# Performance work log

Measured on AMD Instinct MI355X. Metric: run time of the kernel, lower is better.

The kernel has to match this reference:

```python
import jax, jax.numpy as jnp
import numpy as np

SCALE = 8.0  # sqrt(d_head=64), per init_kwargs
B, H, S, D = 2, 16, 2048, 64


def setup_inputs() -> dict:
    key = jax.random.key(0)
    kq, kk, kv = jax.random.split(key, 3)
    q = jax.random.normal(kq, (B, H, S, D), dtype=jnp.float32)
    k = jax.random.normal(kk, (B, H, S, D), dtype=jnp.float32)
    v = jax.random.normal(kv, (B, H, S, D), dtype=jnp.float32)
    # causal mask: True where attention is NOT allowed (strictly upper triangle)
    causal = jnp.triu(jnp.ones((S, S), dtype=bool), k=1)
    mask = jnp.broadcast_to(causal, (B, H, S, S))
    return {"q": q, "k": k, "v": v, "mask": mask}


def reference(q, k, v, mask):
    # score = (q @ k^T) / scale, masked_fill(mask, -inf), softmax, @ v
    score = jnp.einsum('bhqd,bhkd->bhqk', q, k) / SCALE
    score = jnp.where(mask, -jnp.inf, score)
    attn = jax.nn.softmax(score, axis=-1)
    output = jnp.einsum('bhqk,bhkd->bhqd', attn, v)
    return (attn, output)
```

## Files before the change

### kernel.cpp

```cpp
#include <hip/hip_runtime.h>
#include <hip/hip_bf16.h>

#define S_LEN 2048
#define D_HEAD 64
#define SD (S_LEN * D_HEAD)
#define TILE_B 8192
#define NTILES 32

typedef __attribute__((ext_vector_type(8))) short short8;
typedef __attribute__((ext_vector_type(4))) float f32x4;

__device__ __forceinline__ unsigned short f2b(float f) {
  unsigned int u = __float_as_uint(f);
  u += 0x7fffu + ((u >> 16) & 1u);
  return (unsigned short)(u >> 16);
}

__device__ __forceinline__ float b2f(unsigned short s) {
  return __uint_as_float(((unsigned int)s) << 16);
}

__device__ __forceinline__ void gl_lds16(const void* g, void* l) {
  __builtin_amdgcn_global_load_lds(
      (const __attribute__((address_space(1))) unsigned int*)g,
      (__attribute__((address_space(3))) unsigned int*)l, 16, 0, 0);
}

__device__ __forceinline__ void stage8k(const char* gsrc, char* ldst, int w, int lane) {
  gl_lds16(gsrc + ((w * 64 + lane) << 4),        ldst + ((w * 64) << 4));
  gl_lds16(gsrc + ((256 + w * 64 + lane) << 4),  ldst + ((256 + w * 64) << 4));
}

__global__ __launch_bounds__(256) void convert_kv_kernel(
    const float* __restrict__ K, const float* __restrict__ V,
    char* __restrict__ Kpre, char* __restrict__ Vpre) {
  const int bid = blockIdx.x;
  const int tid = threadIdx.x;
  if (bid < 1024) {
    const int bh = bid >> 5, tile = bid & 31;
    const float* Kb = K + (size_t)bh * SD + tile * 64 * 64;
    char* out = Kpre + (size_t)bid * TILE_B;
    #pragma unroll
    for (int j = 0; j < 2; ++j) {
      int c = tid + j * 256;
      int sl = c >> 3;
      int d0 = ((c & 7) ^ (sl & 7)) << 3;
      const float* src = Kb + sl * 64 + d0;
      float4 a = *(const float4*)src;
      float4 b = *(const float4*)(src + 4);
      short8 o;
      o[0]=(short)f2b(a.x); o[1]=(short)f2b(a.y); o[2]=(short)f2b(a.z); o[3]=(short)f2b(a.w);
      o[4]=(short)f2b(b.x); o[5]=(short)f2b(b.y); o[6]=(short)f2b(b.z); o[7]=(short)f2b(b.w);
      *(short8*)(out + c * 16) = o;
    }
  } else {
    __shared__ float Vl[64][65];
    const int vb = bid - 1024;
    const int bh = vb >> 5, tile = vb & 31;
    const float* Vb = V + (size_t)bh * SD + tile * 64 * 64;
    #pragma unroll
    for (int j = 0; j < 4; ++j) {
      int row = (tid >> 4) + j * 16;
      int c4 = (tid & 15) << 2;
      float4 v = *(const float4*)(Vb + row * 64 + c4);
      Vl[row][c4+0] = v.x; Vl[row][c4+1] = v.y; Vl[row][c4+2] = v.z; Vl[row][c4+3] = v.w;
    }
    __syncthreads();
    char* out = Vpre + (size_t)vb * TILE_B;
    #pragma unroll
    for (int j = 0; j < 2; ++j) {
      int c = tid + j * 256;
      int d = c >> 3;
      int s0 = ((c & 7) ^ ((d >> 2) & 7)) << 3;
      short8 o;
      #pragma unroll
      for (int i = 0; i < 8; ++i) o[i] = (short)f2b(Vl[s0 + i][d]);
      *(short8*)(out + c * 16) = o;
    }
  }
}

__global__ __launch_bounds__(256, 4) void sdpa_pre_kernel(
    const float* __restrict__ Qg, const char* __restrict__ Kpre,
    const char* __restrict__ Vpre, float* __restrict__ attn,
    float* __restrict__ outp) {
  const int j  = blockIdx.x >> 8;
  const int rr = blockIdx.x & 255;
  const int xcd = rr & 7;
  const int cu  = rr >> 3;
  const int bh  = xcd + ((cu & 3) << 3);
  const int u   = cu >> 2;
  const int qt  = (j == 0) ? u : (j == 1) ? (15 - u) : (j == 2) ? (16 + u) : (31 - u);

  const int tid = threadIdx.x, wave = tid >> 6, lane = tid & 63;
  const int g = lane >> 4, m = lane & 15;
  const int swzK = (m & 7) << 4;

  __shared__ __align__(16) unsigned short Ring[4][4096];
  __shared__ __align__(16) unsigned short Pl[4][1024];
  char* const RB = (char*)Ring;
  char* const PB = (char*)(&Pl[wave][0]);

  const size_t bhSD = (size_t)bh * SD;
  const size_t bhSS = (size_t)bh << 22;
  const char* KpreBH = Kpre + (size_t)bh * NTILES * TILE_B;
  const char* VpreBH = Vpre + (size_t)bh * NTILES * TILE_B;

  int vro[4], vsz[4];
  #pragma unroll
  for (int dc = 0; dc < 4; ++dc) {
    int d = dc * 16 + m;
    vro[dc] = d << 7;
    vsz[dc] = ((d >> 2) & 7) << 4;
  }
  const float SCL = 0.18033688011112042f;

  const int q0 = qt << 6;
  const int nIt = qt + 1;
  const int qwrow = q0 + wave * 16;
  const int qbase = qwrow + g * 4;

  short8 aq0, aq1;
  {
    const float* qp = Qg + bhSD + (size_t)(qwrow + m) * D_HEAD + g * 8;
    float4 x0 = *(const float4*)(qp);
    float4 x1 = *(const float4*)(qp + 4);
    float4 y0 = *(const float4*)(qp + 32);
    float4 y1 = *(const float4*)(qp + 36);
    aq0[0]=(short)f2b(x0.x*SCL); aq0[1]=(short)f2b(x0.y*SCL);
    aq0[2]=(short)f2b(x0.z*SCL); aq0[3]=(short)f2b(x0.w*SCL);
    aq0[4]=(short)f2b(x1.x*SCL); aq0[5]=(short)f2b(x1.y*SCL);
    aq0[6]=(short)f2b(x1.z*SCL); aq0[7]=(short)f2b(x1.w*SCL);
    aq1[0]=(short)f2b(y0.x*SCL); aq1[1]=(short)f2b(y0.y*SCL);
    aq1[2]=(short)f2b(y0.z*SCL); aq1[3]=(short)f2b(y0.w*SCL);
    aq1[4]=(short)f2b(y1.x*SCL); aq1[5]=(short)f2b(y1.y*SCL);
    aq1[6]=(short)f2b(y1.z*SCL); aq1[7]=(short)f2b(y1.w*SCL);
  }

  float rs0 = 0.f, rs1 = 0.f, rs2 = 0.f, rs3 = 0.f;
  {
    const int npre = nIt < 3 ? nIt : 3;
    for (int t0 = 0; t0 < npre; ++t0)
      stage8k(KpreBH + (size_t)t0 * TILE_B, RB + t0 * TILE_B, wave, lane);
  }
  for (int it = 0; it < nIt; ++it) {
    if (it + 2 < nIt)      { asm volatile("s_waitcnt vmcnt(4)" ::: "memory"); }
    else if (it + 1 < nIt) { asm volatile("s_waitcnt vmcnt(2)" ::: "memory"); }
    else                   { asm volatile("s_waitcnt vmcnt(0)" ::: "memory"); }
    __builtin_amdgcn_s_barrier();
    __builtin_amdgcn_sched_barrier(0);
    if (it + 3 < nIt)
      stage8k(KpreBH + (size_t)(it + 3) * TILE_B, RB + ((it + 3) & 3) * TILE_B, wave, lane);
    asm volatile("" ::: "memory");
    const char* KB = RB + (it & 3) * TILE_B;
    const int kc = it << 6;
    if (kc + 64 <= qwrow) {
      #pragma unroll
      for (int t = 0; t < 4; ++t) {
        f32x4 acc = {0.f, 0.f, 0.f, 0.f};
        const int rb = (t * 16 + m) << 7;
        short8 b0 = *(const short8*)(KB + ((rb + g * 16) ^ swzK));
        short8 b1 = *(const short8*)(KB + ((rb + 64 + g * 16) ^ swzK));
        acc = __builtin_amdgcn_mfma_f32_16x16x32_bf16(aq0, b0, acc, 0, 0, 0);
        acc = __builtin_amdgcn_mfma_f32_16x16x32_bf16(aq1, b1, acc, 0, 0, 0);
        rs0 += exp2f(acc[0]);
        rs1 += exp2f(acc[1]);
        rs2 += exp2f(acc[2]);
        rs3 += exp2f(acc[3]);
      }
    } else {
      #pragma unroll
      for (int t = 0; t < 4; ++t) {
        f32x4 acc = {0.f, 0.f, 0.f, 0.f};
        const int rb = (t * 16 + m) << 7;
        short8 b0 = *(const short8*)(KB + ((rb + g * 16) ^ swzK));
        short8 b1 = *(const short8*)(KB + ((rb + 64 + g * 16) ^ swzK));
        acc = __builtin_amdgcn_mfma_f32_16x16x32_bf16(aq0, b0, acc, 0, 0, 0);
        acc = __builtin_amdgcn_mfma_f32_16x16x32_bf16(aq1, b1, acc, 0, 0, 0);
        const int kcol = kc + t * 16 + m;
        rs0 += (kcol <= qbase + 0) ? exp2f(acc[0]) : 0.f;
        rs1 += (kcol <= qbase + 1) ? exp2f(acc[1]) : 0.f;
        rs2 += (kcol <= qbase + 2) ? exp2f(acc[2]) : 0.f;
        rs3 += (kcol <= qbase + 3) ? exp2f(acc[3]) : 0.f;
      }
    }
  }
  #pragma unroll
  for (int sft = 1; sft < 16; sft <<= 1) {
    rs0 += __shfl_xor(rs0, sft, 64);
    rs1 += __shfl_xor(rs1, sft, 64);
    rs2 += __shfl_xor(rs2, sft, 64);
    rs3 += __shfl_xor(rs3, sft, 64);
  }
  const float ri0 = 1.f / rs0, ri1 = 1.f / rs1, ri2 = 1.f / rs2, ri3 = 1.f / rs3;

  f32x4 o0 = {0.f,0.f,0.f,0.f}, o1 = {0.f,0.f,0.f,0.f};
  f32x4 o2 = {0.f,0.f,0.f,0.f}, o3 = {0.f,0.f,0.f,0.f};
  __builtin_amdgcn_s_barrier();
  stage8k(KpreBH, RB + 0 * TILE_B, wave, lane);
  stage8k(VpreBH, RB + 2 * TILE_B, wave, lane);
  int cur = 0;
  const int r4 = lane >> 4;
  const int cf = (lane & 15) << 2;
  for (int it = 0; it < nIt; ++it) {
    if (it == 0) { asm volatile("s_waitcnt vmcnt(0)" ::: "memory"); }
    else         { asm volatile("s_waitcnt vmcnt(4)" ::: "memory"); }
    __builtin_amdgcn_s_barrier();
    __builtin_amdgcn_sched_barrier(0);
    if (it + 1 < nIt) {
      stage8k(KpreBH + (size_t)(it + 1) * TILE_B, RB + (cur ^ 1) * TILE_B, wave, lane);
      stage8k(VpreBH + (size_t)(it + 1) * TILE_B, RB + (2 + (cur ^ 1)) * TILE_B, wave, lane);
    }
    asm volatile("" ::: "memory");
    const char* KB = RB + cur * TILE_B;
    const char* VB = RB + (2 + cur) * TILE_B;
    const int kc = it << 6;
    if (kc + 64 <= qwrow) {
      #pragma unroll
      for (int t = 0; t < 4; ++t) {
        f32x4 acc = {0.f, 0.f, 0.f, 0.f};
        const int rb = (t * 16 + m) << 7;
        short8 b0 = *(const short8*)(KB + ((rb + g * 16) ^ swzK));
        short8 b1 = *(const short8*)(KB + ((rb + 64 + g * 16) ^ swzK));
        acc = __builtin_amdgcn_mfma_f32_16x16x32_bf16(aq0, b0, acc, 0, 0, 0);
        acc = __builtin_amdgcn_mfma_f32_16x16x32_bf16(aq1, b1, acc, 0, 0, 0);
        float p0 = exp2f(acc[0]) * ri0;
        float p1 = exp2f(acc[1]) * ri1;
        float p2 = exp2f(acc[2]) * ri2;
        float p3 = exp2f(acc[3]) * ri3;
        const int r0 = g * 4, c2 = (t * 16 + m) << 1;
        *(unsigned short*)(PB + ((((r0+0)<<7) + c2) ^ (((r0+0)&7)<<4))) = f2b(p0);
        *(unsigned short*)(PB + ((((r0+1)<<7) + c2) ^ (((r0+1)&7)<<4))) = f2b(p1);
        *(unsigned short*)(PB + ((((r0+2)<<7) + c2) ^ (((r0+2)&7)<<4))) = f2b(p2);
        *(unsigned short*)(PB + ((((r0+3)<<7) + c2) ^ (((r0+3)&7)<<4))) = f2b(p3);
      }
    } else {
      #pragma unroll
      for (int t = 0; t < 4; ++t) {
        f32x4 acc = {0.f, 0.f, 0.f, 0.f};
        const int rb = (t * 16 + m) << 7;
        short8 b0 = *(const short8*)(KB + ((rb + g * 16) ^ swzK));
        short8 b1 = *(const short8*)(KB + ((rb + 64 + g * 16) ^ swzK));
        acc = __builtin_amdgcn_mfma_f32_16x16x32_bf16(aq0, b0, acc, 0, 0, 0);
        acc = __builtin_amdgcn_mfma_f32_16x16x32_bf16(aq1, b1, acc, 0, 0, 0);
        const int kcol = kc + t * 16 + m;
        float p0 = (kcol <= qbase + 0) ? exp2f(acc[0]) * ri0 : 0.f;
        float p1 = (kcol <= qbase + 1) ? exp2f(acc[1]) * ri1 : 0.f;
        float p2 = (kcol <= qbase + 2) ? exp2f(acc[2]) * ri2 : 0.f;
        float p3 = (kcol <= qbase + 3) ? exp2f(acc[3]) * ri3 : 0.f;
        const int r0 = g * 4, c2 = (t * 16 + m) << 1;
        *(unsigned short*)(PB + ((((r0+0)<<7) + c2) ^ (((r0+0)&7)<<4))) = f2b(p0);
        *(unsigned short*)(PB + ((((r0+1)<<7) + c2) ^ (((r0+1)&7)<<4))) = f2b(p1);
        *(unsigned short*)(PB + ((((r0+2)<<7) + c2) ^ (((r0+2)&7)<<4))) = f2b(p2);
        *(unsigned short*)(PB + ((((r0+3)<<7) + c2) ^ (((r0+3)&7)<<4))) = f2b(p3);
      }
    }
    {
      float* abase2 = attn + bhSS + (size_t)qwrow * S_LEN + kc;
      #pragma unroll
      for (int jj = 0; jj < 4; ++jj) {
        const int row = 4 * jj + r4;
        const int off = (((row << 7) + (cf << 1))) ^ ((row & 7) << 4);
        ushort4 pr = *(const ushort4*)(PB + off);
        float4 fa;
        fa.x = b2f(pr.x); fa.y = b2f(pr.y); fa.z = b2f(pr.z); fa.w = b2f(pr.w);
        *(float4*)(abase2 + (size_t)row * S_LEN + cf) = fa;
      }
    }
    short8 pa0 = *(const short8*)(PB + (((m << 7) + g * 16) ^ swzK));
    short8 pa1 = *(const short8*)(PB + (((m << 7) + 64 + g * 16) ^ swzK));
    #pragma unroll
    for (int dc = 0; dc < 4; ++dc) {
      short8 bv0 = *(const short8*)(VB + ((vro[dc] + g * 16) ^ vsz[dc]));
      short8 bv1 = *(const short8*)(VB + ((vro[dc] + 64 + g * 16) ^ vsz[dc]));
      f32x4& od = (dc == 0) ? o0 : (dc == 1) ? o1 : (dc == 2) ? o2 : o3;
      od = __builtin_amdgcn_mfma_f32_16x16x32_bf16(pa0, bv0, od, 0, 0, 0);
      od = __builtin_amdgcn_mfma_f32_16x16x32_bf16(pa1, bv1, od, 0, 0, 0);
    }
    cur ^= 1;
  }

  #pragma unroll
  for (int reg = 0; reg < 4; ++reg) {
    float* op = outp + bhSD + (size_t)(qbase + reg) * D_HEAD + m;
    op[ 0] = o0[reg];
    op[16] = o1[reg];
    op[32] = o2[reg];
    op[48] = o3[reg];
  }

  const int col0 = nIt << 6;
  const int nvec = (S_LEN - col0) >> 2;
  if (nvec > 0) {
    const float4 z = {0.f, 0.f, 0.f, 0.f};
    for (int r = 0; r < 64; ++r) {
      float4* rp = (float4*)(attn + bhSS + (size_t)(q0 + r) * S_LEN + col0);
      for (int i = tid; i < nvec; i += 256) rp[i] = z;
    }
  }
}

__global__ __launch_bounds__(256) void sdpa_fb_kernel(
    const float* __restrict__ Qg, const float* __restrict__ Kg,
    const float* __restrict__ Vg, float* __restrict__ attn,
    float* __restrict__ outp) {
  const int bh = blockIdx.x >> 4;
  const int pi = blockIdx.x & 15;
  const int tid  = threadIdx.x;
  const int wave = tid >> 6;
  const int lane = tid & 63;
  const int g = lane >> 4;
  const int m = lane & 15;
  const int swzK = (m & 7) << 4;
  __shared__ __align__(16) unsigned short Kl[2][64 * 64];
  __shared__ __align__(16) unsigned short Vt[2][64 * 64];
  __shared__ __align__(16) unsigned short Pl[4][16 * 64];
  char* const PB = (char*)(&Pl[wave][0]);
  const size_t bhSD = (size_t)bh * (S_LEN * D_HEAD);
  const size_t bhSS = (size_t)bh * ((size_t)S_LEN * S_LEN);
  int ss[4], dd[4], koff[4];
  #pragma unroll
  for (int j = 0; j < 4; ++j) {
    int f = tid + j * 256;
    ss[j] = f >> 4;
    dd[j] = (f & 15) << 2;
    koff[j] = (((ss[j] << 6) + dd[j]) << 1) ^ ((ss[j] & 7) << 4);
  }
  int vro[4], vsz[4];
  #pragma unroll
  for (int dc = 0; dc < 4; ++dc) {
    int d = dc * 16 + m;
    vro[dc] = d << 7;
    vsz[dc] = ((d >> 2) & 7) << 4;
  }
  const float SCL = 0.18033688011112042f;
  for (int sidx = 0; sidx < 2; ++sidx) {
    const int qt = sidx ? (31 - pi) : pi;
    const int q0 = qt << 6;
    const int kmax = q0 + 64;
    const int nIter = kmax >> 6;
    const int qwrow = q0 + wave * 16;
    const int qbase = qwrow + g * 4;
    short8 aq0, aq1;
    {
      const float* qp = Qg + bhSD + (size_t)(qwrow + m) * D_HEAD + g * 8;
      float4 x0 = *(const float4*)(qp);
      float4 x1 = *(const float4*)(qp + 4);
      float4 y0 = *(const float4*)(qp + 32);
      float4 y1 = *(const float4*)(qp + 36);
      aq0[0]=(short)f2b(x0.x*SCL); aq0[1]=(short)f2b(x0.y*SCL);
      aq0[2]=(short)f2b(x0.z*SCL); aq0[3]=(short)f2b(x0.w*SCL);
      aq0[4]=(short)f2b(x1.x*SCL); aq0[5]=(short)f2b(x1.y*SCL);
      aq0[6]=(short)f2b(x1.z*SCL); aq0[7]=(short)f2b(x1.w*SCL);
      aq1[0]=(short)f2b(y0.x*SCL); aq1[1]=(short)f2b(y0.y*SCL);
      aq1[2]=(short)f2b(y0.z*SCL); aq1[3]=(short)f2b(y0.w*SCL);
      aq1[4]=(short)f2b(y1.x*SCL); aq1[5]=(short)f2b(y1.y*SCL);
      aq1[6]=(short)f2b(y1.z*SCL); aq1[7]=(short)f2b(y1.w*SCL);
    }
    float rs0 = 0.f, rs1 = 0.f, rs2 = 0.f, rs3 = 0.f;
    {
      float4 kr[4];
      #pragma unroll
      for (int j = 0; j < 4; ++j)
        kr[j] = *(const float4*)(Kg + bhSD + (size_t)ss[j] * D_HEAD + dd[j]);
      #pragma unroll
      for (int j = 0; j < 4; ++j) {
        ushort4 kb;
        kb.x = f2b(kr[j].x); kb.y = f2b(kr[j].y);
        kb.z = f2b(kr[j].z); kb.w = f2b(kr[j].w);
        *(ushort4*)((char*)Kl[0] + koff[j]) = kb;
      }
    }
    __syncthreads();
    int cur = 0;
    for (int it = 0; it < nIter; ++it) {
      const int kc = it << 6;
      const bool pf = (it + 1 < nIter);
      float4 kr[4];
      if (pf) {
        #pragma unroll
        for (int j = 0; j < 4; ++j)
          kr[j] = *(const float4*)(Kg + bhSD + (size_t)(kc + 64 + ss[j]) * D_HEAD + dd[j]);
      }
      const char* KB = (const char*)Kl[cur];
      #pragma unroll
      for (int t = 0; t < 4; ++t) {
        f32x4 acc = {0.f, 0.f, 0.f, 0.f};
        const int rb = (t * 16 + m) << 7;
        short8 b0 = *(const short8*)(KB + ((rb + g * 16) ^ swzK));
        short8 b1 = *(const short8*)(KB + ((rb + 64 + g * 16) ^ swzK));
        acc = __builtin_amdgcn_mfma_f32_16x16x32_bf16(aq0, b0, acc, 0, 0, 0);
        acc = __builtin_amdgcn_mfma_f32_16x16x32_bf16(aq1, b1, acc, 0, 0, 0);
        const int kcol = kc + t * 16 + m;
        rs0 += (kcol <= qbase + 0) ? exp2f(acc[0]) : 0.f;
        rs1 += (kcol <= qbase + 1) ? exp2f(acc[1]) : 0.f;
        rs2 += (kcol <= qbase + 2) ? exp2f(acc[2]) : 0.f;
        rs3 += (kcol <= qbase + 3) ? exp2f(acc[3]) : 0.f;
      }
      if (pf) {
        #pragma unroll
        for (int j = 0; j < 4; ++j) {
          ushort4 kb;
          kb.x = f2b(kr[j].x); kb.y = f2b(kr[j].y);
          kb.z = f2b(kr[j].z); kb.w = f2b(kr[j].w);
          *(ushort4*)((char*)Kl[cur ^ 1] + koff[j]) = kb;
        }
      }
      __syncthreads();
      cur ^= 1;
    }
    #pragma unroll
    for (int sft = 1; sft < 16; sft <<= 1) {
      rs0 += __shfl_xor(rs0, sft, 64);
      rs1 += __shfl_xor(rs1, sft, 64);
      rs2 += __shfl_xor(rs2, sft, 64);
      rs3 += __shfl_xor(rs3, sft, 64);
    }
    const float ri0 = 1.f / rs0, ri1 = 1.f / rs1, ri2 = 1.f / rs2, ri3 = 1.f / rs3;
    f32x4 o0 = {0.f,0.f,0.f,0.f}, o1 = {0.f,0.f,0.f,0.f};
    f32x4 o2 = {0.f,0.f,0.f,0.f}, o3 = {0.f,0.f,0.f,0.f};
    {
      float4 kr[4], vr[4];
      #pragma unroll
      for (int j = 0; j < 4; ++j) {
        kr[j] = *(const float4*)(Kg + bhSD + (size_t)ss[j] * D_HEAD + dd[j]);
        vr[j] = *(const float4*)(Vg + bhSD + (size_t)ss[j] * D_HEAD + dd[j]);
      }
      #pragma unroll
      for (int j = 0; j < 4; ++j) {
        ushort4 kb;
        kb.x = f2b(kr[j].x); kb.y = f2b(kr[j].y);
        kb.z = f2b(kr[j].z); kb.w = f2b(kr[j].w);
        *(ushort4*)((char*)Kl[0] + koff[j]) = kb;
        const int d0 = dd[j], s2 = ss[j] << 1;
        char* VB1 = (char*)Vt[0];
        *(unsigned short*)(VB1 + ((((d0+0)<<7) + s2) ^ ((((d0+0)>>2)&7)<<4))) = f2b(vr[j].x);
        *(unsigned short*)(VB1 + ((((d0+1)<<7) + s2) ^ ((((d0+1)>>2)&7)<<4))) = f2b(vr[j].y);
        *(unsigned short*)(VB1 + ((((d0+2)<<7) + s2) ^ ((((d0+2)>>2)&7)<<4))) = f2b(vr[j].z);
        *(unsigned short*)(VB1 + ((((d0+3)<<7) + s2) ^ ((((d0+3)>>2)&7)<<4))) = f2b(vr[j].w);
      }
    }
    __syncthreads();
    cur = 0;
    for (int it = 0; it < nIter; ++it) {
      const int kc = it << 6;
      const bool pf = (it + 1 < nIter);
      float4 kr[4], vr[4];
      if (pf) {
        #pragma unroll
        for (int j = 0; j < 4; ++j) {
          kr[j] = *(const float4*)(Kg + bhSD + (size_t)(kc + 64 + ss[j]) * D_HEAD + dd[j]);
          vr[j] = *(const float4*)(Vg + bhSD + (size_t)(kc + 64 + ss[j]) * D_HEAD + dd[j]);
        }
      }
      const char* KB = (const char*)Kl[cur];
      const char* VB = (const char*)Vt[cur];
      float* arow = attn + bhSS + (size_t)qbase * S_LEN + kc;
      #pragma unroll
      for (int t = 0; t < 4; ++t) {
        f32x4 acc = {0.f, 0.f, 0.f, 0.f};
        const int rb = (t * 16 + m) << 7;
        short8 b0 = *(const short8*)(KB + ((rb + g * 16) ^ swzK));
        short8 b1 = *(const short8*)(KB + ((rb + 64 + g * 16) ^ swzK));
        acc = __builtin_amdgcn_mfma_f32_16x16x32_bf16(aq0, b0, acc, 0, 0, 0);
        acc = __builtin_amdgcn_mfma_f32_16x16x32_bf16(aq1, b1, acc, 0, 0, 0);
        const int kcol = kc + t * 16 + m;
        const int tc = t * 16 + m;
        float p0 = (kcol <= qbase + 0) ? exp2f(acc[0]) * ri0 : 0.f;
        float p1 = (kcol <= qbase + 1) ? exp2f(acc[1]) * ri1 : 0.f;
        float p2 = (kcol <= qbase + 2) ? exp2f(acc[2]) * ri2 : 0.f;
        float p3 = (kcol <= qbase + 3) ? exp2f(acc[3]) * ri3 : 0.f;
        arow[0 * S_LEN + tc] = p0;
        arow[1 * S_LEN + tc] = p1;
        arow[2 * S_LEN + tc] = p2;
        arow[3 * S_LEN + tc] = p3;
        const int r0 = g * 4, c2 = tc << 1;
        *(unsigned short*)(PB + ((((r0+0)<<7) + c2) ^ (((r0+0)&7)<<4))) = f2b(p0);
        *(unsigned short*)(PB + ((((r0+1)<<7) + c2) ^ (((r0+1)&7)<<4))) = f2b(p1);
        *(unsigned short*)(PB + ((((r0+2)<<7) + c2) ^ (((r0+2)&7)<<4))) = f2b(p2);
        *(unsigned short*)(PB + ((((r0+3)<<7) + c2) ^ (((r0+3)&7)<<4))) = f2b(p3);
      }
      short8 pa0 = *(const short8*)(PB + (((m << 7) + g * 16) ^ swzK));
      short8 pa1 = *(const short8*)(PB + (((m << 7) + 64 + g * 16) ^ swzK));
      #pragma unroll
      for (int dc = 0; dc < 4; ++dc) {
        short8 bv0 = *(const short8*)(VB + ((vro[dc] + g * 16) ^ vsz[dc]));
        short8 bv1 = *(const short8*)(VB + ((vro[dc] + 64 + g * 16) ^ vsz[dc]));
        f32x4& od = (dc == 0) ? o0 : (dc == 1) ? o1 : (dc == 2) ? o2 : o3;
        od = __builtin_amdgcn_mfma_f32_16x16x32_bf16(pa0, bv0, od, 0, 0, 0);
        od = __builtin_amdgcn_mfma_f32_16x16x32_bf16(pa1, bv1, od, 0, 0, 0);
      }
      if (pf) {
        #pragma unroll
        for (int j = 0; j < 4; ++j) {
          ushort4 kb;
          kb.x = f2b(kr[j].x); kb.y = f2b(kr[j].y);
          kb.z = f2b(kr[j].z); kb.w = f2b(kr[j].w);
          *(ushort4*)((char*)Kl[cur ^ 1] + koff[j]) = kb;
          const int d0 = dd[j], s2 = ss[j] << 1;
          char* VB1 = (char*)Vt[cur ^ 1];
          *(unsigned short*)(VB1 + ((((d0+0)<<7) + s2) ^ ((((d0+0)>>2)&7)<<4))) = f2b(vr[j].x);
          *(unsigned short*)(VB1 + ((((d0+1)<<7) + s2) ^ ((((d0+1)>>2)&7)<<4))) = f2b(vr[j].y);
          *(unsigned short*)(VB1 + ((((d0+2)<<7) + s2) ^ ((((d0+2)>>2)&7)<<4))) = f2b(vr[j].z);
          *(unsigned short*)(VB1 + ((((d0+3)<<7) + s2) ^ ((((d0+3)>>2)&7)<<4))) = f2b(vr[j].w);
        }
      }
      __syncthreads();
      cur ^= 1;
    }
    #pragma unroll
    for (int reg = 0; reg < 4; ++reg) {
      float* op = outp + bhSD + (size_t)(qbase + reg) * D_HEAD + m;
      op[ 0] = o0[reg];
      op[16] = o1[reg];
      op[32] = o2[reg];
      op[48] = o3[reg];
    }
    const int ncols = S_LEN - kmax;
    if (ncols > 0) {
      const float4 z = {0.f, 0.f, 0.f, 0.f};
      const int nvec = ncols >> 2;
      for (int r = 0; r < 64; ++r) {
        float4* rp = (float4*)(attn + bhSS + (size_t)(q0 + r) * S_LEN + kmax);
        for (int i = tid; i < nvec; i += 256) rp[i] = z;
      }
    }
  }
}

extern "C" void kernel_launch(void* const* d_in, const int* in_sizes, int n_in,
                              void* d_out, int out_size, void* d_ws, size_t ws_size,
                              hipStream_t stream) {
  (void)in_sizes; (void)n_in; (void)out_size;
  const float* q = (const float*)d_in[0];
  const float* k = (const float*)d_in[1];
  const float* v = (const float*)d_in[2];
  float* attn = (float*)d_out;
  float* outp = attn + (size_t)2 * 16 * 2048 * 2048;
  const size_t pre_bytes = (size_t)32 * NTILES * TILE_B;
  if (ws_size >= 2 * pre_bytes) {
    char* Kpre = (char*)d_ws;
    char* Vpre = Kpre + pre_bytes;
    convert_kv_kernel<<<2048, 256, 0, stream>>>(k, v, Kpre, Vpre);
    sdpa_pre_kernel<<<1024, 256, 0, stream>>>(q, Kpre, Vpre, attn, outp);
  } else {
    sdpa_fb_kernel<<<512, 256, 0, stream>>>(q, k, v, attn, outp);
  }
}
```

Before: 168.6 us.

## Read K directly from global memory in row-sum pass instead of LDS ring

The first (softmax denominator) pass now loads pre-swizzled K fragments straight from global memory into registers, with precomputed per-lane offsets and a 2x unrolled loop. This drops the 4-slot LDS ring, the vmcnt waits and the workgroup barriers from that pass. The second pass keeps LDS double buffering, now in separate K and V arrays. The risk is exposed global/L2 latency without explicit prefetch, plus uncoalesced 16-byte per-lane loads repeated by all four waves.

```diff
diff --git a/kernel.cpp b/kernel.cpp
--- a/kernel.cpp
+++ b/kernel.cpp
@@ -96,9 +96,9 @@
   const int g = lane >> 4, m = lane & 15;
   const int swzK = (m & 7) << 4;
 
-  __shared__ __align__(16) unsigned short Ring[4][4096];
+  __shared__ __align__(16) unsigned short Kl[2][4096];
+  __shared__ __align__(16) unsigned short Vt[2][4096];
   __shared__ __align__(16) unsigned short Pl[4][1024];
-  char* const RB = (char*)Ring;
   char* const PB = (char*)(&Pl[wave][0]);
 
   const size_t bhSD = (size_t)bh * SD;
@@ -137,32 +137,28 @@
     aq1[6]=(short)f2b(y1.z*SCL); aq1[7]=(short)f2b(y1.w*SCL);
   }
 
+  int koffs[8];
+  #pragma unroll
+  for (int tt = 0; tt < 4; ++tt) {
+    const int s = tt * 16 + m;
+    const int sw = (s & 7) << 4;
+    koffs[2 * tt]     = (s << 7) + ((g * 16) ^ sw);
+    koffs[2 * tt + 1] = (s << 7) + ((64 + g * 16) ^ sw);
+  }
   float rs0 = 0.f, rs1 = 0.f, rs2 = 0.f, rs3 = 0.f;
-  {
-    const int npre = nIt < 3 ? nIt : 3;
-    for (int t0 = 0; t0 < npre; ++t0)
-      stage8k(KpreBH + (size_t)t0 * TILE_B, RB + t0 * TILE_B, wave, lane);
-  }
+  #pragma unroll 2
   for (int it = 0; it < nIt; ++it) {
-    if (it + 2 < nIt)      { asm volatile("s_waitcnt vmcnt(4)" ::: "memory"); }
-    else if (it + 1 < nIt) { asm volatile("s_waitcnt vmcnt(2)" ::: "memory"); }
-    else                   { asm volatile("s_waitcnt vmcnt(0)" ::: "memory"); }
-    __builtin_amdgcn_s_barrier();
-    __builtin_amdgcn_sched_barrier(0);
-    if (it + 3 < nIt)
-      stage8k(KpreBH + (size_t)(it + 3) * TILE_B, RB + ((it + 3) & 3) * TILE_B, wave, lane);
-    asm volatile("" ::: "memory");
-    const char* KB = RB + (it & 3) * TILE_B;
+    const char* TB = KpreBH + (size_t)it * TILE_B;
+    short8 cb[8];
+    #pragma unroll
+    for (int j2 = 0; j2 < 8; ++j2) cb[j2] = *(const short8*)(TB + koffs[j2]);
     const int kc = it << 6;
     if (kc + 64 <= qwrow) {
       #pragma unroll
       for (int t = 0; t < 4; ++t) {
         f32x4 acc = {0.f, 0.f, 0.f, 0.f};
-        const int rb = (t * 16 + m) << 7;
-        short8 b0 = *(const short8*)(KB + ((rb + g * 16) ^ swzK));
-        short8 b1 = *(const short8*)(KB + ((rb + 64 + g * 16) ^ swzK));
-        acc = __builtin_amdgcn_mfma_f32_16x16x32_bf16(aq0, b0, acc, 0, 0, 0);
-        acc = __builtin_amdgcn_mfma_f32_16x16x32_bf16(aq1, b1, acc, 0, 0, 0);
+        acc = __builtin_amdgcn_mfma_f32_16x16x32_bf16(aq0, cb[2 * t], acc, 0, 0, 0);
+        acc = __builtin_amdgcn_mfma_f32_16x16x32_bf16(aq1, cb[2 * t + 1], acc, 0, 0, 0);
         rs0 += exp2f(acc[0]);
         rs1 += exp2f(acc[1]);
         rs2 += exp2f(acc[2]);
@@ -172,11 +168,8 @@
       #pragma unroll
       for (int t = 0; t < 4; ++t) {
         f32x4 acc = {0.f, 0.f, 0.f, 0.f};
-        const int rb = (t * 16 + m) << 7;
-        short8 b0 = *(const short8*)(KB + ((rb + g * 16) ^ swzK));
-        short8 b1 = *(const short8*)(KB + ((rb + 64 + g * 16) ^ swzK));
-        acc = __builtin_amdgcn_mfma_f32_16x16x32_bf16(aq0, b0, acc, 0, 0, 0);
-        acc = __builtin_amdgcn_mfma_f32_16x16x32_bf16(aq1, b1, acc, 0, 0, 0);
+        acc = __builtin_amdgcn_mfma_f32_16x16x32_bf16(aq0, cb[2 * t], acc, 0, 0, 0);
+        acc = __builtin_amdgcn_mfma_f32_16x16x32_bf16(aq1, cb[2 * t + 1], acc, 0, 0, 0);
         const int kcol = kc + t * 16 + m;
         rs0 += (kcol <= qbase + 0) ? exp2f(acc[0]) : 0.f;
         rs1 += (kcol <= qbase + 1) ? exp2f(acc[1]) : 0.f;
@@ -196,9 +189,8 @@
 
   f32x4 o0 = {0.f,0.f,0.f,0.f}, o1 = {0.f,0.f,0.f,0.f};
   f32x4 o2 = {0.f,0.f,0.f,0.f}, o3 = {0.f,0.f,0.f,0.f};
-  __builtin_amdgcn_s_barrier();
-  stage8k(KpreBH, RB + 0 * TILE_B, wave, lane);
-  stage8k(VpreBH, RB + 2 * TILE_B, wave, lane);
+  stage8k(KpreBH, (char*)Kl[0], wave, lane);
+  stage8k(VpreBH, (char*)Vt[0], wave, lane);
   int cur = 0;
   const int r4 = lane >> 4;
   const int cf = (lane & 15) << 2;
@@ -208,12 +200,12 @@
     __builtin_amdgcn_s_barrier();
     __builtin_amdgcn_sched_barrier(0);
     if (it + 1 < nIt) {
-      stage8k(KpreBH + (size_t)(it + 1) * TILE_B, RB + (cur ^ 1) * TILE_B, wave, lane);
-      stage8k(VpreBH + (size_t)(it + 1) * TILE_B, RB + (2 + (cur ^ 1)) * TILE_B, wave, lane);
+      stage8k(KpreBH + (size_t)(it + 1) * TILE_B, (char*)Kl[cur ^ 1], wave, lane);
+      stage8k(VpreBH + (size_t)(it + 1) * TILE_B, (char*)Vt[cur ^ 1], wave, lane);
     }
     asm volatile("" ::: "memory");
-    const char* KB = RB + cur * TILE_B;
-    const char* VB = RB + (2 + cur) * TILE_B;
+    const char* KB = (const char*)Kl[cur];
+    const char* VB = (const char*)Vt[cur];
     const int kc = it << 6;
     if (kc + 64 <= qwrow) {
       #pragma unroll
```

Result: no change. 170.4 us (+1.1%).
